# Kernel tuning notes

Hardware: AMD Instinct MI355X
Metric: run time of the kernel (lower is better)

Reference implementation:

```python
import jax, jax.numpy as jnp
import numpy as np

D_MODEL = 1024
NUM_HEADS = 16
HEAD_DIM = D_MODEL // NUM_HEADS
CAUSAL = True


def rope_cos_sin(seq_len, dim):
    inv_freq = 1.0 / (10000.0 ** (jnp.arange(0, dim, 2, dtype=jnp.float32) / dim))
    t = jnp.arange(seq_len, dtype=jnp.float32)
    freqs = jnp.einsum('i,j->ij', t, inv_freq)          # [S, dim/2]
    emb = jnp.concatenate([freqs, freqs], axis=-1)      # [S, dim]
    return jnp.cos(emb), jnp.sin(emb)


def rotate_half(x):
    x1, x2 = jnp.split(x, 2, axis=-1)
    return jnp.concatenate([-x2, x1], axis=-1)


def setup_inputs() -> dict:
    key = jax.random.key(0)
    k1, k2, k3, k4, k5 = jax.random.split(key, 5)
    B, S = 2, 2048
    x = jax.random.normal(k1, (B, S, D_MODEL), dtype=jnp.float32)
    s = 1.0 / np.sqrt(D_MODEL)
    W_qkv = jax.random.normal(k2, (D_MODEL, 3 * D_MODEL), dtype=jnp.float32) * s
    b_qkv = jax.random.normal(k3, (3 * D_MODEL,), dtype=jnp.float32) * 0.01
    W_out = jax.random.normal(k4, (D_MODEL, D_MODEL), dtype=jnp.float32) * s
    b_out = jax.random.normal(k5, (D_MODEL,), dtype=jnp.float32) * 0.01
    return {"x": x, "W_qkv": W_qkv, "b_qkv": b_qkv, "W_out": W_out, "b_out": b_out}


def reference(x, W_qkv, b_qkv, W_out, b_out):
    B, S, _ = x.shape
    qkv = x @ W_qkv + b_qkv                              # [B, S, 3D]
    q, k, v = jnp.split(qkv, 3, axis=-1)
    # [B, H, S, hd]
    q = q.reshape(B, S, NUM_HEADS, HEAD_DIM).transpose(0, 2, 1, 3)
    k = k.reshape(B, S, NUM_HEADS, HEAD_DIM).transpose(0, 2, 1, 3)
    v = v.reshape(B, S, NUM_HEADS, HEAD_DIM).transpose(0, 2, 1, 3)
    cos, sin = rope_cos_sin(S, HEAD_DIM)                 # [S, hd]
    cos = cos[None, None]
    sin = sin[None, None]
    q = q * cos + rotate_half(q) * sin
    k = k * cos + rotate_half(k) * sin
    scores = jnp.einsum('bhqd,bhkd->bhqk', q, k) / np.sqrt(HEAD_DIM)
    if CAUSAL:
        causal_mask = jnp.triu(jnp.ones((S, S), dtype=bool), k=1)
        scores = jnp.where(causal_mask, -jnp.inf, scores)
    attn = jax.nn.softmax(scores, axis=-1)
    out = jnp.einsum('bhqk,bhkd->bhqd', attn, v)         # [B, H, S, hd]
    out = out.transpose(0, 2, 1, 3).reshape(B, S, D_MODEL)
    return out @ W_out + b_out
```

## Files before the change

### kernel.cpp

```cpp
#include <hip/hip_runtime.h>
#include <hip/hip_bf16.h>
#include <math.h>

typedef __bf16 bf16;
typedef __bf16 bf16x8 __attribute__((ext_vector_type(8)));
typedef unsigned short ushort8 __attribute__((ext_vector_type(8)));
typedef float floatx4 __attribute__((ext_vector_type(4)));

#define MFMA_BF16(a, b, c) __builtin_amdgcn_mfma_f32_16x16x32_bf16(a, b, c, 0, 0, 0)

#define Q_SCALE 0.18033688011112042f
#define NEG_INVFREQ_LOG2 0.41524101186092029f
#define INV_2PI 0.15915494309189535f

#if __has_builtin(__builtin_amdgcn_exp2f)
#define EXP2F(x) __builtin_amdgcn_exp2f(x)
#else
#define EXP2F(x) exp2f(x)
#endif

__device__ __forceinline__ void hw_sincos_rev(float rev, float* sn, float* cs) {
#if __has_builtin(__builtin_amdgcn_sinf) && __has_builtin(__builtin_amdgcn_cosf) && \
    __has_builtin(__builtin_amdgcn_fractf)
  const float f = __builtin_amdgcn_fractf(rev);
  *sn = __builtin_amdgcn_sinf(f);
  *cs = __builtin_amdgcn_cosf(f);
#else
  sincosf(rev * 6.2831853071795864f, sn, cs);
#endif
}

__device__ __forceinline__ bf16x8 cvt8(const float4 a, const float4 b) {
  bf16x8 t;
  t[0] = (bf16)a.x; t[1] = (bf16)a.y; t[2] = (bf16)a.z; t[3] = (bf16)a.w;
  t[4] = (bf16)b.x; t[5] = (bf16)b.y; t[6] = (bf16)b.z; t[7] = (bf16)b.w;
  return t;
}

__device__ __forceinline__ unsigned int pack2(float a, float b) {
#if __has_builtin(__builtin_amdgcn_cvt_pk_bf16_f32)
  return __builtin_bit_cast(unsigned int, __builtin_amdgcn_cvt_pk_bf16_f32(a, b));
#else
  unsigned short lo = __builtin_bit_cast(unsigned short, (bf16)a);
  unsigned short hi = __builtin_bit_cast(unsigned short, (bf16)b);
  return (unsigned int)lo | ((unsigned int)hi << 16);
#endif
}

__device__ __forceinline__ void gld16(const bf16* g, bf16* l) {
  __builtin_amdgcn_global_load_lds(
      (const __attribute__((address_space(1))) unsigned int*)g,
      (__attribute__((address_space(3))) unsigned int*)l, 16, 0, 0);
}

__device__ __forceinline__ int swz_stage_col(int lane) {
  return ((lane & 3) ^ (((lane >> 2) + (lane >> 4)) & 3)) * 8;
}
__device__ __forceinline__ int swz_read_col(int quad, int c) {
  return (quad ^ ((c + (c >> 2)) & 3)) * 8;
}

__device__ __forceinline__ int xcd_swz(int lin, int n) {
  return (lin & 7) * (n >> 3) + (lin >> 3);
}

__device__ __forceinline__ void transpose_tile(const float* __restrict__ in,
                                               bf16* __restrict__ out, int N,
                                               int K, int n0, int k0, int t,
                                               bf16 (*T)[40]) {
  {
    const int k = t >> 3, n8 = (t & 7) * 8;
    const float* p = &in[(size_t)(k0 + k) * N + n0 + n8];
    const float4 a = *(const float4*)p;
    const float4 b = *(const float4*)(p + 4);
    const float v[8] = {a.x, a.y, a.z, a.w, b.x, b.y, b.z, b.w};
#pragma unroll
    for (int j = 0; j < 8; j++) {
      const int n = n8 + j;
      T[n][k ^ (8 * ((n >> 3) & 3))] = (bf16)v[j];
    }
  }
  __syncthreads();
  {
    const int n = t >> 2, k8 = (t & 3) * 8;
    const int kp = k8 ^ (8 * ((n >> 3) & 3));
    *(bf16x8*)&out[(size_t)(n0 + n) * K + k0 + k8] = *(const bf16x8*)&T[n][kp];
  }
}

__global__ __launch_bounds__(256) void prep_kernel(
    const float* __restrict__ x, bf16* __restrict__ xb,
    const float* __restrict__ Wqkv, bf16* __restrict__ Wqkvt,
    const float* __restrict__ Wout, bf16* __restrict__ Wot) {
  __shared__ __align__(16) bf16 T[64][40];
  const int b = blockIdx.x, t = threadIdx.x;
  if (b < 2048) {
    const int i = b * 256 + t;
    const float4 a = *(const float4*)&x[(size_t)i * 8];
    const float4 d = *(const float4*)&x[(size_t)i * 8 + 4];
    *(bf16x8*)&xb[(size_t)i * 8] = cvt8(a, d);
  } else if (b < 3584) {
    const int idx = b - 2048;
    transpose_tile(Wqkv, Wqkvt, 3072, 1024, (idx % 48) * 64, (idx / 48) * 32, t,
                   T);
  } else {
    const int idx = b - 3584;
    transpose_tile(Wout, Wot, 1024, 1024, (idx % 16) * 64, (idx / 16) * 32, t,
                   T);
  }
}

template <int TN, int MODE>
__global__ __launch_bounds__(256) void gemm_kernel(
    const bf16* __restrict__ A, const bf16* __restrict__ Bt,
    const float* __restrict__ bias, void* __restrict__ out0,
    bf16* __restrict__ outK, bf16* __restrict__ outV, int M, int N, int K) {
  constexpr int NI = TN / 32;
  constexpr int BI = TN / 32;
  __shared__ __align__(16) bf16 As2[2][128][32];
  __shared__ __align__(16) bf16 Bs2[2][TN][32];

  const int tid = threadIdx.x, lane = tid & 63, w = tid >> 6;
  const int c = lane & 15, quad = lane >> 4;
  const int wm = w >> 1, wn = w & 1;
  const int m0 = blockIdx.y * 128, n0 = blockIdx.x * TN;
  const int srow = lane >> 2, scol = swz_stage_col(lane);
  const int rcol = swz_read_col(quad, c);

  floatx4 acc[4][NI] = {};

  for (int k0 = 0; k0 < K; k0 += 64) {
    __syncthreads();
#pragma unroll
    for (int i = 0; i < 4; i++) {
      const int seg = w * 4 + i;
      const int kh = seg >> 3, r0 = (seg & 7) * 16;
      gld16(&A[(size_t)(m0 + r0 + srow) * K + k0 + kh * 32 + scol],
            &As2[kh][r0][0]);
    }
#pragma unroll
    for (int i = 0; i < BI; i++) {
      const int seg = w * BI + i;
      const int kh = seg / (TN / 16), r0 = (seg % (TN / 16)) * 16;
      gld16(&Bt[(size_t)(n0 + r0 + srow) * K + k0 + kh * 32 + scol],
            &Bs2[kh][r0][0]);
    }
    __syncthreads();

#pragma unroll
    for (int kh = 0; kh < 2; kh++) {
      bf16x8 af[4], bfr[NI];
#pragma unroll
      for (int mi = 0; mi < 4; mi++)
        af[mi] = *(const bf16x8*)&As2[kh][wm * 64 + mi * 16 + c][rcol];
#pragma unroll
      for (int ni = 0; ni < NI; ni++)
        bfr[ni] = *(const bf16x8*)&Bs2[kh][wn * (TN / 2) + ni * 16 + c][rcol];
#pragma unroll
      for (int mi = 0; mi < 4; mi++)
#pragma unroll
        for (int ni = 0; ni < NI; ni++)
          acc[mi][ni] = MFMA_BF16(af[mi], bfr[ni], acc[mi][ni]);
    }
  }

  if (MODE == 0) {
#pragma unroll
    for (int mi = 0; mi < 4; mi++)
#pragma unroll
      for (int ni = 0; ni < NI; ni++)
#pragma unroll
        for (int r = 0; r < 4; r++) {
          const int row = m0 + wm * 64 + mi * 16 + quad * 4 + r;
          const int col = n0 + wn * (TN / 2) + ni * 16 + c;
          ((float*)out0)[(size_t)row * N + col] = acc[mi][ni][r] + bias[col];
        }
  } else {
    const int colb = n0 + wn * (TN / 2);
    const int t = colb >> 10;
    const int h = (colb & 1023) >> 6;
    bf16* dst = (t == 0) ? (bf16*)out0 : (t == 1 ? outK : outV);
    if (t == 2) {
#pragma unroll
      for (int ni = 0; ni < NI; ni++) {
        const int d = ni * 16 + c;
        const float bv = bias[colb + ni * 16 + c];
#pragma unroll
        for (int mi = 0; mi < 4; mi++) {
          const int row = m0 + wm * 64 + mi * 16 + quad * 4;
          const int b = row >> 11, s = row & 2047;
          const uint2 u = {pack2(acc[mi][ni][0] + bv, acc[mi][ni][1] + bv),
                           pack2(acc[mi][ni][2] + bv, acc[mi][ni][3] + bv)};
          *(uint2*)&dst[(((size_t)b * 16 + h) * 64 + d) * 2048 + s] = u;
        }
      }
    } else {
      const float qs = (t == 0) ? Q_SCALE : 1.0f;
      const float invr[2] = {exp2f(-NEG_INVFREQ_LOG2 * (float)c) * INV_2PI,
                             exp2f(-NEG_INVFREQ_LOG2 * (float)(16 + c)) * INV_2PI};
#pragma unroll
      for (int mi = 0; mi < 4; mi++) {
#pragma unroll
        for (int r = 0; r < 4; r++) {
          const int row = m0 + wm * 64 + mi * 16 + quad * 4 + r;
          const int b = row >> 11, s = row & 2047;
          const size_t base = (((size_t)b * 16 + h) * 2048 + s) * 64;
#pragma unroll
          for (int ni = 0; ni < 2; ni++) {
            float sn, cs;
            hw_sincos_rev((float)s * invr[ni], &sn, &cs);
            const float v1 = acc[mi][ni][r] + bias[colb + ni * 16 + c];
            const float v2 = acc[mi][ni + 2][r] + bias[colb + (ni + 2) * 16 + c];
            const int d = ni * 16 + c;
            dst[base + d] = (bf16)((v1 * cs - v2 * sn) * qs);
            dst[base + d + 32] = (bf16)((v2 * cs + v1 * sn) * qs);
          }
        }
      }
    }
  }
}

struct AttnState {
  floatx4 o[4];
  floatx4 l;
};

__device__ __forceinline__ void attn_step(
    const bf16x8 qf[2], const bf16x8 kf[4][2], const bf16x8 vf[4][2],
    const bf16x8 ones, bf16 (*PsW)[72], AttnState& st, int qglob, int kbase,
    bool diag, int c, int quad) {
  floatx4 sacc[4] = {};
#pragma unroll
  for (int kg = 0; kg < 4; kg++)
#pragma unroll
    for (int dh = 0; dh < 2; dh++)
      sacc[kg] = MFMA_BF16(kf[kg][dh], qf[dh], sacc[kg]);

#pragma unroll
  for (int kg = 0; kg < 4; kg++) {
    float p[4];
#pragma unroll
    for (int r = 0; r < 4; r++) {
      float e = EXP2F(sacc[kg][r]);
      if (diag && (kbase + kg * 16 + quad * 4 + r > qglob)) e = 0.0f;
      p[r] = e;
    }
    const uint2 u = {pack2(p[0], p[1]), pack2(p[2], p[3])};
    *(uint2*)&PsW[c][kg * 16 + quad * 4] = u;
  }

  bf16x8 pf[2];
#pragma unroll
  for (int ks = 0; ks < 2; ks++)
    pf[ks] = *(const bf16x8*)&PsW[c][ks * 32 + quad * 8];

#pragma unroll
  for (int dg = 0; dg < 4; dg++)
#pragma unroll
    for (int ks = 0; ks < 2; ks++)
      st.o[dg] = MFMA_BF16(vf[dg][ks], pf[ks], st.o[dg]);
  st.l = MFMA_BF16(ones, pf[0], st.l);
  st.l = MFMA_BF16(ones, pf[1], st.l);
}

__global__ __launch_bounds__(256) void attn_kernel(const bf16* __restrict__ Q,
                                                   const bf16* __restrict__ K,
                                                   const bf16* __restrict__ V,
                                                   bf16* __restrict__ Aout) {
  const int S = 2048;
  int p, bh;
  {
    const int n = gridDim.x * gridDim.y;
    const int swz = xcd_swz(blockIdx.x + gridDim.x * blockIdx.y, n);
    p = swz % gridDim.x;
    bh = swz / gridDim.x;
  }
  const int tid = threadIdx.x, lane = tid & 63, wave = tid >> 6;
  const int c = lane & 15, quad = lane >> 4;

  __shared__ __align__(16) bf16 Ks2[2][2][64][32];
  __shared__ __align__(16) bf16 Vt[2][64][64];
  __shared__ __align__(16) bf16 Ps[4][2][16][72];

  const bf16* Qb = Q + (size_t)bh * S * 64;
  const bf16* Kb = K + (size_t)bh * S * 64;
  const bf16* Vb = V + (size_t)bh * S * 64;
  const int b = bh >> 4, h = bh & 15;

  const int qA = p, qB = 31 - p;
  const int qgA = qA * 64 + wave * 16 + c;
  const int qgB = qB * 64 + wave * 16 + c;

  bf16x8 qfA[2], qfB[2];
#pragma unroll
  for (int dh = 0; dh < 2; dh++) {
    qfA[dh] = *(const bf16x8*)&Qb[(size_t)qgA * 64 + dh * 32 + quad * 8];
    qfB[dh] = *(const bf16x8*)&Qb[(size_t)qgB * 64 + dh * 32 + quad * 8];
  }

  bf16x8 ones;
#pragma unroll
  for (int j = 0; j < 8; j++) ones[j] = (bf16)1.0f;

  AttnState stA = {}, stB = {};

  const int ksr = lane >> 2, ksc = swz_stage_col(lane);
  const int krcol = swz_read_col(quad, c);
  const int vd = lane >> 3;
  const int vg = lane & 7;

  auto stage = [&](int bb, int kt) {
    const int kt64 = kt * 64;
#pragma unroll
    for (int i = 0; i < 2; i++) {
      const int seg = wave * 2 + i;
      const int dh = seg >> 2, r0 = (seg & 3) * 16;
      gld16(&Kb[(size_t)(kt64 + r0 + ksr) * 64 + dh * 32 + ksc],
            &Ks2[bb][dh][r0][0]);
    }
#pragma unroll
    for (int i = 0; i < 2; i++) {
      const int d0 = wave * 16 + i * 8;
      const int dd = d0 + vd;
      const int g = vg ^ (dd & 7);
      gld16(&Vb[(size_t)dd * 2048 + kt64 + g * 8], &Vt[bb][d0][0]);
    }
  };

  stage(0, 0);
  __syncthreads();

  int buf = 0;
  for (int kt = 0; kt <= qB; kt++) {
    if (kt < qB) stage(buf ^ 1, kt + 1);

    bf16x8 kf[4][2];
#pragma unroll
    for (int kg = 0; kg < 4; kg++)
#pragma unroll
      for (int dh = 0; dh < 2; dh++)
        kf[kg][dh] = *(const bf16x8*)&Ks2[buf][dh][kg * 16 + c][krcol];

    bf16x8 vf[4][2];
#pragma unroll
    for (int dg = 0; dg < 4; dg++) {
      const int d = dg * 16 + c;
#pragma unroll
      for (int ks = 0; ks < 2; ks++) {
        const int g = (ks * 4 + quad) ^ (c & 7);
        vf[dg][ks] = *(const bf16x8*)&Vt[buf][d][g * 8];
      }
    }

    attn_step(qfB, kf, vf, ones, Ps[wave][0], stB, qgB, kt * 64, kt == qB, c,
              quad);
    if (kt <= qA)
      attn_step(qfA, kf, vf, ones, Ps[wave][1], stA, qgA, kt * 64, kt == qA, c,
                quad);

    __syncthreads();
    buf ^= 1;
  }

  const float ivA = 1.0f / stA.l[0], ivB = 1.0f / stB.l[0];

#pragma unroll
  for (int dg = 0; dg < 4; dg++) {
    const uint2 uA = {pack2(stA.o[dg][0] * ivA, stA.o[dg][1] * ivA),
                      pack2(stA.o[dg][2] * ivA, stA.o[dg][3] * ivA)};
    const uint2 uB = {pack2(stB.o[dg][0] * ivB, stB.o[dg][1] * ivB),
                      pack2(stB.o[dg][2] * ivB, stB.o[dg][3] * ivB)};
    *(uint2*)&Aout[((size_t)b * 2048 + qgA) * 1024 + h * 64 + dg * 16 + quad * 4] = uA;
    *(uint2*)&Aout[((size_t)b * 2048 + qgB) * 1024 + h * 64 + dg * 16 + quad * 4] = uB;
  }
}

extern "C" void kernel_launch(void* const* d_in, const int* in_sizes, int n_in,
                              void* d_out, int out_size, void* d_ws,
                              size_t ws_size, hipStream_t stream) {
  const float* x = (const float*)d_in[0];
  const float* W_qkv = (const float*)d_in[1];
  const float* b_qkv = (const float*)d_in[2];
  const float* W_out = (const float*)d_in[3];
  const float* b_out = (const float*)d_in[4];
  float* out = (float*)d_out;

  const int B = 2, S = 2048, NH = 16;
  const size_t qn = (size_t)B * NH * S * 64;

  bf16* xb = (bf16*)d_ws;
  bf16* Wqkvt = xb + qn;
  bf16* Wot = Wqkvt + 3072 * 1024;
  bf16* Qw = Wot + 1024 * 1024;
  bf16* Kw = Qw + qn;
  bf16* Vw = Kw + qn;
  bf16* AO = xb;

  prep_kernel<<<dim3(4096), 256, 0, stream>>>(x, xb, W_qkv, Wqkvt, W_out, Wot);

  gemm_kernel<128, 1><<<dim3(3072 / 128, 4096 / 128), 256, 0, stream>>>(
      xb, Wqkvt, b_qkv, Qw, Kw, Vw, 4096, 3072, 1024);
  attn_kernel<<<dim3(16, B * NH), 256, 0, stream>>>(Qw, Kw, Vw, AO);
  gemm_kernel<64, 0><<<dim3(1024 / 64, 4096 / 128), 256, 0, stream>>>(
      AO, Wot, b_out, out, nullptr, nullptr, 4096, 1024, 1024);
}
```

Baseline: 192.3 us.

## Split paired query tiles across two wave groups in 512-thread attention blocks

The attention kernel now launches 512 threads per block. Waves 0-3 process the late query tile (qB) and waves 4-7 process the early tile (qA), where before each wave processed both tiles one after the other. K/V staging is spread over 8 waves, one load each, and the P scratch buffer is indexed per wave. The aim is more parallel waves and less serial work and register pressure per wave. The cost is an imbalance: the qA group idles at the shared barriers once its tile is finished while the qB group keeps iterating.

```diff
diff --git a/kernel.cpp b/kernel.cpp
--- a/kernel.cpp
+++ b/kernel.cpp
@@ -264,7 +264,7 @@
   st.l = MFMA_BF16(ones, pf[1], st.l);
 }
 
-__global__ __launch_bounds__(256) void attn_kernel(const bf16* __restrict__ Q,
+__global__ __launch_bounds__(512) void attn_kernel(const bf16* __restrict__ Q,
                                                    const bf16* __restrict__ K,
                                                    const bf16* __restrict__ V,
                                                    bf16* __restrict__ Aout) {
@@ -278,10 +278,11 @@
   }
   const int tid = threadIdx.x, lane = tid & 63, wave = tid >> 6;
   const int c = lane & 15, quad = lane >> 4;
+  const int grp = wave >> 2, w4 = wave & 3;
 
   __shared__ __align__(16) bf16 Ks2[2][2][64][32];
   __shared__ __align__(16) bf16 Vt[2][64][64];
-  __shared__ __align__(16) bf16 Ps[4][2][16][72];
+  __shared__ __align__(16) bf16 Ps[8][16][72];
 
   const bf16* Qb = Q + (size_t)bh * S * 64;
   const bf16* Kb = K + (size_t)bh * S * 64;
@@ -289,21 +290,19 @@
   const int b = bh >> 4, h = bh & 15;
 
   const int qA = p, qB = 31 - p;
-  const int qgA = qA * 64 + wave * 16 + c;
-  const int qgB = qB * 64 + wave * 16 + c;
-
-  bf16x8 qfA[2], qfB[2];
-#pragma unroll
-  for (int dh = 0; dh < 2; dh++) {
-    qfA[dh] = *(const bf16x8*)&Qb[(size_t)qgA * 64 + dh * 32 + quad * 8];
-    qfB[dh] = *(const bf16x8*)&Qb[(size_t)qgB * 64 + dh * 32 + quad * 8];
-  }
+  const int qtile = (grp == 0) ? qB : qA;
+  const int qg = qtile * 64 + w4 * 16 + c;
+
+  bf16x8 qf[2];
+#pragma unroll
+  for (int dh = 0; dh < 2; dh++)
+    qf[dh] = *(const bf16x8*)&Qb[(size_t)qg * 64 + dh * 32 + quad * 8];
 
   bf16x8 ones;
 #pragma unroll
   for (int j = 0; j < 8; j++) ones[j] = (bf16)1.0f;
 
-  AttnState stA = {}, stB = {};
+  AttnState st = {};
 
   const int ksr = lane >> 2, ksc = swz_stage_col(lane);
   const int krcol = swz_read_col(quad, c);
@@ -312,67 +311,62 @@
 
   auto stage = [&](int bb, int kt) {
     const int kt64 = kt * 64;
-#pragma unroll
-    for (int i = 0; i < 2; i++) {
-      const int seg = wave * 2 + i;
+    {
+      const int seg = wave;
       const int dh = seg >> 2, r0 = (seg & 3) * 16;
       gld16(&Kb[(size_t)(kt64 + r0 + ksr) * 64 + dh * 32 + ksc],
             &Ks2[bb][dh][r0][0]);
     }
-#pragma unroll
-    for (int i = 0; i < 2; i++) {
-      const int d0 = wave * 16 + i * 8;
+    {
+      const int d0 = wave * 8;
       const int dd = d0 + vd;
       const int g = vg ^ (dd & 7);
       gld16(&Vb[(size_t)dd * 2048 + kt64 + g * 8], &Vt[bb][d0][0]);
     }
   };
 
+  auto load_kf = [&](int bb, bf16x8 (*kf)[2]) {
+#pragma unroll
+    for (int kg = 0; kg < 4; kg++)
+#pragma unroll
+      for (int dh = 0; dh < 2; dh++)
+        kf[kg][dh] = *(const bf16x8*)&Ks2[bb][dh][kg * 16 + c][krcol];
+  };
+  auto load_vf = [&](int bb, bf16x8 (*vf)[2]) {
+#pragma unroll
+    for (int dg = 0; dg < 4; dg++) {
+      const int d = dg * 16 + c;
+#pragma unroll
+      for (int ks = 0; ks < 2; ks++) {
+        const int g = (ks * 4 + quad) ^ (c & 7);
+        vf[dg][ks] = *(const bf16x8*)&Vt[bb][d][g * 8];
+      }
+    }
+  };
+
   stage(0, 0);
   __syncthreads();
 
   int buf = 0;
   for (int kt = 0; kt <= qB; kt++) {
     if (kt < qB) stage(buf ^ 1, kt + 1);
-
-    bf16x8 kf[4][2];
-#pragma unroll
-    for (int kg = 0; kg < 4; kg++)
-#pragma unroll
-      for (int dh = 0; dh < 2; dh++)
-        kf[kg][dh] = *(const bf16x8*)&Ks2[buf][dh][kg * 16 + c][krcol];
-
-    bf16x8 vf[4][2];
-#pragma unroll
-    for (int dg = 0; dg < 4; dg++) {
-      const int d = dg * 16 + c;
-#pragma unroll
-      for (int ks = 0; ks < 2; ks++) {
-        const int g = (ks * 4 + quad) ^ (c & 7);
-        vf[dg][ks] = *(const bf16x8*)&Vt[buf][d][g * 8];
-      }
-    }
-
-    attn_step(qfB, kf, vf, ones, Ps[wave][0], stB, qgB, kt * 64, kt == qB, c,
-              quad);
-    if (kt <= qA)
-      attn_step(qfA, kf, vf, ones, Ps[wave][1], stA, qgA, kt * 64, kt == qA, c,
+    if (grp == 0 || kt <= qA) {
+      bf16x8 kf[4][2], vf[4][2];
+      load_kf(buf, kf);
+      load_vf(buf, vf);
+      attn_step(qf, kf, vf, ones, Ps[wave], st, qg, kt * 64, kt == qtile, c,
                 quad);
-
+    }
     __syncthreads();
     buf ^= 1;
   }
 
-  const float ivA = 1.0f / stA.l[0], ivB = 1.0f / stB.l[0];
-
+  const float iv = 1.0f / st.l[0];
 #pragma unroll
   for (int dg = 0; dg < 4; dg++) {
-    const uint2 uA = {pack2(stA.o[dg][0] * ivA, stA.o[dg][1] * ivA),
-                      pack2(stA.o[dg][2] * ivA, stA.o[dg][3] * ivA)};
-    const uint2 uB = {pack2(stB.o[dg][0] * ivB, stB.o[dg][1] * ivB),
-                      pack2(stB.o[dg][2] * ivB, stB.o[dg][3] * ivB)};
-    *(uint2*)&Aout[((size_t)b * 2048 + qgA) * 1024 + h * 64 + dg * 16 + quad * 4] = uA;
-    *(uint2*)&Aout[((size_t)b * 2048 + qgB) * 1024 + h * 64 + dg * 16 + quad * 4] = uB;
+    const uint2 u = {pack2(st.o[dg][0] * iv, st.o[dg][1] * iv),
+                     pack2(st.o[dg][2] * iv, st.o[dg][3] * iv)};
+    *(uint2*)&Aout[((size_t)b * 2048 + qg) * 1024 + h * 64 + dg * 16 + quad * 4] = u;
   }
 }
 
@@ -401,7 +395,7 @@
 
   gemm_kernel<128, 1><<<dim3(3072 / 128, 4096 / 128), 256, 0, stream>>>(
       xb, Wqkvt, b_qkv, Qw, Kw, Vw, 4096, 3072, 1024);
-  attn_kernel<<<dim3(16, B * NH), 256, 0, stream>>>(Qw, Kw, Vw, AO);
+  attn_kernel<<<dim3(16, B * NH), 512, 0, stream>>>(Qw, Kw, Vw, AO);
   gemm_kernel<64, 0><<<dim3(1024 / 64, 4096 / 128), 256, 0, stream>>>(
       AO, Wot, b_out, out, nullptr, nullptr, 4096, 1024, 1024);
 }
```

New measurement: 189.7 us. Within noise of the previous version (-1.4%).
